# Kernel tuning notes

Measured on AMD Instinct MI355X. Metric: run time of the kernel, lower is better.

Reference implementation:

```python
import jax, jax.numpy as jnp
import numpy as np

T, B, V, NG, H, MLP = 1024, 128, 128, 10, 1024, 128
F = V + NG  # feature_size = alphabet one-hot + genre one-hot


def setup_inputs() -> dict:
    key = jax.random.key(0)
    ks = jax.random.split(key, 14)
    s = 0.02
    inp = {
        "x": jax.random.normal(ks[0], (T, B, F), dtype=jnp.float32),
        # LSTMCell 1: input F -> hidden H (PyTorch layout: W_ih [4H, F], W_hh [4H, H])
        "W_ih1": jax.random.normal(ks[1], (4 * H, F), dtype=jnp.float32) * s,
        "b_ih1": jax.random.normal(ks[2], (4 * H,), dtype=jnp.float32) * s,
        "W_hh1": jax.random.normal(ks[3], (4 * H, H), dtype=jnp.float32) * s,
        "b_hh1": jax.random.normal(ks[4], (4 * H,), dtype=jnp.float32) * s,
        # LSTMCell 2: H -> H
        "W_ih2": jax.random.normal(ks[5], (4 * H, H), dtype=jnp.float32) * s,
        "b_ih2": jax.random.normal(ks[6], (4 * H,), dtype=jnp.float32) * s,
        "W_hh2": jax.random.normal(ks[7], (4 * H, H), dtype=jnp.float32) * s,
        "b_hh2": jax.random.normal(ks[8], (4 * H,), dtype=jnp.float32) * s,
        # MLP head: Linear(H,128) -> SELU -> Linear(128, V). Dropout(0.2) is identity in eval.
        "W1": jax.random.normal(ks[9], (MLP, H), dtype=jnp.float32) * s,
        "b1": jax.random.normal(ks[10], (MLP,), dtype=jnp.float32) * s,
        "W2": jax.random.normal(ks[11], (V, MLP), dtype=jnp.float32) * s,
        "b2": jax.random.normal(ks[12], (V,), dtype=jnp.float32) * s,
        "predict": 0,
    }
    return inp


def _lstm_cell(xt, h, c, W_ih, b_ih, W_hh, b_hh):
    # PyTorch LSTMCell gate order: input, forget, cell(g), output
    gates = xt @ W_ih.T + b_ih + h @ W_hh.T + b_hh  # [B, 4H]
    i, f, g, o = jnp.split(gates, 4, axis=-1)
    i, f, o = jax.nn.sigmoid(i), jax.nn.sigmoid(f), jax.nn.sigmoid(o)
    g = jnp.tanh(g)
    c_new = f * c + i * g
    h_new = o * jnp.tanh(c_new)
    return h_new, c_new


def reference(x, W_ih1, b_ih1, W_hh1, b_hh1, W_ih2, b_ih2, W_hh2, b_hh2,
              W1, b1, W2, b2, predict):
    n = x.shape[1]
    h0 = jnp.zeros((n, H), dtype=jnp.float32)
    init = (h0, h0, h0, h0)  # h_t, c_t, h2_t, c2_t

    def step(carry, xt):
        h, c, h2, c2 = carry
        h, c = _lstm_cell(xt, h, c, W_ih1, b_ih1, W_hh1, b_hh1)
        h2, c2 = _lstm_cell(h, h2, c2, W_ih2, b_ih2, W_hh2, b_hh2)
        out = jax.nn.selu(h2 @ W1.T + b1) @ W2.T + b2  # [B, V]
        return (h, c, h2, c2), out

    _, outputs = jax.lax.scan(step, init, x)  # [T, B, V]
    return outputs
```

## Files before the change

### kernel.cpp

```cpp
#include <hip/hip_runtime.h>
#include <cstdint>
#include <cstddef>

#define TT   1024
#define BB   128
#define FEAT 138
#define FPAD 160
#define HH   1024
#define VV   128
#define MM   128
#define K1   1184
#define K1P  1280
#define K2   2048
#define HCH  1024
#define H1N  131072
#define MIDN 16384
#define PKM1 1032
#define PKM2 136
#define OFF_RED 0
#define OFF_WM  32768
#define OFF_H   65792
#define OFF_M   67840
#define LDSZ    68864

typedef __bf16 bf16x8 __attribute__((ext_vector_type(8)));
typedef float  f32x4  __attribute__((ext_vector_type(4)));
typedef unsigned short u16;

__device__ __forceinline__ u16 f2bf(float f) {
  uint32_t u = __float_as_uint(f);
  u += 0x7fffu + ((u >> 16) & 1u);
  return (u16)(u >> 16);
}
__device__ __forceinline__ float sigm(float x) { return 1.0f / (1.0f + __expf(-x)); }
__device__ __forceinline__ float tanh_(float x) {
  float e = __expf(-2.0f * fabsf(x));
  float t = (1.0f - e) / (1.0f + e);
  return x < 0.0f ? -t : t;
}

__device__ __forceinline__ bf16x8 ldcc8(const u16* p) {
  union { unsigned long long q[2]; bf16x8 v; } u;
  const unsigned long long* p64 = (const unsigned long long*)p;
  u.q[0] = __hip_atomic_load(p64,     __ATOMIC_RELAXED, __HIP_MEMORY_SCOPE_AGENT);
  u.q[1] = __hip_atomic_load(p64 + 1, __ATOMIC_RELAXED, __HIP_MEMORY_SCOPE_AGENT);
  return u.v;
}
__device__ __forceinline__ void stcc16(u16* p, uint4 v) {
  unsigned long long* p64 = (unsigned long long*)p;
  unsigned long long lo = ((unsigned long long)v.y << 32) | v.x;
  unsigned long long hi = ((unsigned long long)v.w << 32) | v.z;
  __hip_atomic_store(p64,     lo, __ATOMIC_RELAXED, __HIP_MEMORY_SCOPE_AGENT);
  __hip_atomic_store(p64 + 1, hi, __ATOMIC_RELAXED, __HIP_MEMORY_SCOPE_AGENT);
}

__global__ void conv_w1i(const float* __restrict__ Wih, const float* __restrict__ Whh,
                         const float* __restrict__ bi, const float* __restrict__ bh,
                         u16* __restrict__ dst, float* __restrict__ bsum) {
  int rp = blockIdx.x;
  int hc = rp >> 2, g = rp & 3;
  int sr = g * HH + hc;
  if (threadIdx.x == 0) bsum[rp] = bi[sr] + bh[sr];
  for (int k = threadIdx.x; k < K1P; k += 256) {
    float v = 0.0f;
    if (k < FPAD)    v = (k < FEAT) ? Wih[(size_t)sr * FEAT + k] : 0.0f;
    else if (k < K1) v = Whh[(size_t)sr * HH + (k - FPAD)];
    dst[(size_t)rp * K1P + k] = f2bf(v);
  }
}
__global__ void conv_w2i(const float* __restrict__ Wih, const float* __restrict__ Whh,
                         const float* __restrict__ bi, const float* __restrict__ bh,
                         u16* __restrict__ dst, float* __restrict__ bsum) {
  int rp = blockIdx.x;
  int hc = rp >> 2, g = rp & 3;
  int sr = g * HH + hc;
  if (threadIdx.x == 0) bsum[rp] = bi[sr] + bh[sr];
  for (int k = threadIdx.x; k < K2; k += 256) {
    float v = (k < HH) ? Wih[(size_t)sr * HH + k] : Whh[(size_t)sr * HH + (k - HH)];
    dst[(size_t)rp * K2 + k] = f2bf(v);
  }
}
__global__ void conv_mlpw(const float* __restrict__ W1, const float* __restrict__ W2,
                          u16* __restrict__ A, u16* __restrict__ Bm) {
  int i = blockIdx.x * 256 + threadIdx.x;
  if (i < MM * HH) A[i] = f2bf(W1[i]);
  else {
    int j = i - MM * HH;
    if (j < VV * MM) Bm[j] = f2bf(W2[j]);
  }
}
__global__ void conv_x(const float* __restrict__ x, u16* __restrict__ Xb) {
  int blk = blockIdx.x;
  int t = blk / 20, c = blk % 20;
  int b = threadIdx.x;
  if (b >= BB) return;
  const float* src = x + ((size_t)t * BB + b) * FEAT;
  u16 v[8];
#pragma unroll
  for (int e = 0; e < 8; ++e) {
    int col = c * 8 + e;
    v[e] = (col < FEAT) ? f2bf(src[col]) : (u16)0;
  }
  *(uint4*)(Xb + (((size_t)t * 20 + c) * BB + b) * 8) = *(uint4*)v;
}
__global__ void zero_ws(uint4* __restrict__ p, int n16) {
  int i = blockIdx.x * 256 + threadIdx.x;
  if (i < n16) p[i] = uint4{0, 0, 0, 0};
}


__device__ __forceinline__ void mac_step(const bf16x8& a0, const bf16x8& a1,
                                         const u16* __restrict__ bptr,
                                         f32x4 (&acc)[2][4]) {
  bf16x8 Bf[4];
#pragma unroll
  for (int n = 0; n < 4; ++n) Bf[n] = *(const bf16x8*)(bptr + n * 128);
#pragma unroll
  for (int n = 0; n < 4; ++n) {
    acc[0][n] = __builtin_amdgcn_mfma_f32_16x16x32_bf16(a0, Bf[n], acc[0][n], 0, 0, 0);
    acc[1][n] = __builtin_amdgcn_mfma_f32_16x16x32_bf16(a1, Bf[n], acc[1][n], 0, 0, 0);
  }
}

__device__ __forceinline__ void ld_tile_cc(const u16* bptr, bf16x8 (&B)[4]) {
#pragma unroll
  for (int n = 0; n < 4; ++n) B[n] = ldcc8(bptr + n * 128);
}
__device__ __forceinline__ void mfma_tile(const bf16x8& a0, const bf16x8& a1,
                                          const bf16x8 (&B)[4], f32x4 (&acc)[2][4]) {
#pragma unroll
  for (int n = 0; n < 4; ++n) {
    acc[0][n] = __builtin_amdgcn_mfma_f32_16x16x32_bf16(a0, B[n], acc[0][n], 0, 0, 0);
    acc[1][n] = __builtin_amdgcn_mfma_f32_16x16x32_bf16(a1, B[n], acc[1][n], 0, 0, 0);
  }
}
template<int NT, int OFS, int NA>
__device__ __forceinline__ void mac_ring_cc(const bf16x8 (&A0)[NA], const bf16x8 (&A1)[NA],
                                            const u16* __restrict__ bp,
                                            f32x4 (&acc)[2][4]) {
  constexpr int D = NT < 4 ? NT : 4;
  bf16x8 Bq[D][4];
#pragma unroll
  for (int s = 0; s < D; ++s) ld_tile_cc(bp + (size_t)s * 4096, Bq[s]);
#pragma unroll
  for (int s = 0; s < NT; ++s) {
    mfma_tile(A0[OFS + s], A1[OFS + s], Bq[s % D], acc);
    if (s + D < NT) ld_tile_cc(bp + (size_t)(s + D) * 4096, Bq[s % D]);
  }
}

__device__ __forceinline__ void red_write(float* __restrict__ rg,
                                          const f32x4 (&acc)[2][4], int lane) {
#pragma unroll
  for (int mt = 0; mt < 2; ++mt)
#pragma unroll
    for (int n = 0; n < 4; ++n)
      *(f32x4*)(rg + (mt * 4 + n) * 256 + lane * 4) = acc[mt][n];
}
__device__ __forceinline__ void red_add(const float* __restrict__ rg,
                                        f32x4 (&acc)[2][4], int lane) {
#pragma unroll
  for (int mt = 0; mt < 2; ++mt)
#pragma unroll
    for (int n = 0; n < 4; ++n)
      acc[mt][n] += *(const f32x4*)(rg + (mt * 4 + n) * 256 + lane * 4);
}

__device__ __forceinline__ void lstm_tail(f32x4 (&acc)[2][4], const f32x4& bsv0,
                                          const f32x4& bsv1, float (&cst)[2][4],
                                          char* smem, int bh, int lane, int q, int l16,
                                          u16* __restrict__ houtChunk) {
  u16* st = (u16*)(smem + OFF_H) + bh * 512;
#pragma unroll
  for (int mt = 0; mt < 2; ++mt) {
    const f32x4 bsv = mt ? bsv1 : bsv0;
#pragma unroll
    for (int n = 0; n < 4; ++n) {
      float iv = sigm(acc[mt][n][0] + bsv[0]);
      float fv = sigm(acc[mt][n][1] + bsv[1]);
      float gv = tanh_(acc[mt][n][2] + bsv[2]);
      float ov = sigm(acc[mt][n][3] + bsv[3]);
      float c = fv * cst[mt][n] + iv * gv;
      cst[mt][n] = c;
      st[(n * 16 + l16) * 8 + mt * 4 + q] = f2bf(ov * tanh_(c));
    }
  }
  uint4 hv4 = *(uint4*)((u16*)(smem + OFF_H) + bh * 512 + lane * 8);
  stcc16(houtChunk + ((size_t)bh * 64 + lane) * 8, hv4);
}

__device__ __forceinline__ void gbar(unsigned* __restrict__ bar, unsigned g) {
  asm volatile("s_waitcnt vmcnt(0)" ::: "memory");
  __syncthreads();
  if (threadIdx.x == 0) {
    unsigned v = __hip_atomic_fetch_add(&bar[(blockIdx.x & 7) * 16], 1u,
                                        __ATOMIC_RELAXED, __HIP_MEMORY_SCOPE_AGENT);
    if (v == 32u * g - 1u) {
      unsigned w = __hip_atomic_fetch_add(&bar[128], 1u,
                                          __ATOMIC_RELAXED, __HIP_MEMORY_SCOPE_AGENT);
      if (w == 8u * g - 1u)
        __hip_atomic_store(&bar[144], g, __ATOMIC_RELAXED, __HIP_MEMORY_SCOPE_AGENT);
    }
    while (__hip_atomic_load(&bar[144], __ATOMIC_RELAXED,
                             __HIP_MEMORY_SCOPE_AGENT) < g)
      __builtin_amdgcn_s_sleep(8);
  }
  __syncthreads();
}

__global__ __launch_bounds__(512, 2) void fused_lstm(
    const u16* __restrict__ W1i, const u16* __restrict__ W2i,
    const u16* __restrict__ W1m, const u16* __restrict__ W2m,
    const u16* __restrict__ Xb, u16* __restrict__ h1b, u16* __restrict__ h2b,
    u16* __restrict__ midb,
    const float* __restrict__ bs1, const float* __restrict__ bs2,
    const float* __restrict__ bm1, const float* __restrict__ bm2,
    float* __restrict__ out, unsigned* __restrict__ bar)
{
  extern __shared__ char smem[];
  const int tid = threadIdx.x, bid = blockIdx.x;
  const int w = tid >> 6, lane = tid & 63, q = lane >> 4, l16 = lane & 15;
  const int kw = w & 3, bh = w >> 2;
  const bool isL1 = bid < 128;
  const int j = isL1 ? bid : bid - 128;
  float* red = (float*)(smem + OFF_RED);
  u16* Wm = (u16*)(smem + OFF_WM);

  float cst[2][4] = {{0, 0, 0, 0}, {0, 0, 0, 0}};
  f32x4 bsv0 = {0, 0, 0, 0}, bsv1 = {0, 0, 0, 0};
  if (kw == 0) {
    const float* bs = isL1 ? bs1 : bs2;
    bsv0 = *(const f32x4*)(bs + (j * 8 + q) * 4);
    bsv1 = *(const f32x4*)(bs + (j * 8 + 4 + q) * 4);
  }

  if (isL1) {
    bf16x8 A1[2][10];
#pragma unroll
    for (int mt = 0; mt < 2; ++mt)
#pragma unroll
      for (int s = 0; s < 10; ++s)
        A1[mt][s] = *(const bf16x8*)(W1i + (size_t)(j * 32 + mt * 16 + l16) * K1P +
                                     (size_t)(kw * 10 + s) * 32 + q * 8);
    if (j < 64) {
      int m0 = (j & 7) * 16;
      for (int i = tid; i < 16 * 128; i += 512) {
        int r = i >> 7, c8 = i & 127;
        *(uint4*)(Wm + r * PKM1 + c8 * 8) =
            *(const uint4*)(W1m + ((size_t)(m0 + r)) * HH + c8 * 8);
      }
    } else {
      int v0 = ((j - 64) & 7) * 16;
      for (int i = tid; i < 16 * 16; i += 512) {
        int r = i >> 4, c8 = i & 15;
        *(uint4*)(Wm + r * PKM2 + c8 * 8) =
            *(const uint4*)(W2m + ((size_t)(v0 + r)) * MM + c8 * 8);
      }
    }
    f32x4 bmv = {0, 0, 0, 0};
    if (w == 3) {
      if (j < 64) bmv = *(const f32x4*)(bm1 + (j & 7) * 16 + q * 4);
      else        bmv = *(const f32x4*)(bm2 + ((j - 64) & 7) * 16 + q * 4);
    }
    __syncthreads();

    for (int p = 0; p < TT + 3; ++p) {
      const bool act = p < TT;
      if (act) {
        const u16* h1p = h1b + (size_t)((p - 1) & 1) * H1N;
        f32x4 acc[2][4];
#pragma unroll
        for (int mt = 0; mt < 2; ++mt)
#pragma unroll
          for (int n = 0; n < 4; ++n) acc[mt][n] = (f32x4){0, 0, 0, 0};
        if (kw == 0) {
          const u16* bx = Xb + (size_t)p * 20480 +
                          ((size_t)q * 128 + bh * 64 + l16) * 8;
#pragma unroll
          for (int s = 0; s < 5; ++s)
            mac_step(A1[0][s], A1[1][s], bx + (size_t)s * 4096, acc);
          const u16* bp = h1p + ((size_t)q * 128 + bh * 64 + l16) * 8;
          mac_ring_cc<5, 5, 10>(A1[0], A1[1], bp, acc);
        } else {
          const u16* bp = h1p + ((size_t)((kw * 10 - 5) * 4 + q) * 128 +
                                 bh * 64 + l16) * 8;
          mac_ring_cc<10, 0, 10>(A1[0], A1[1], bp, acc);
        }
        if (kw >= 2) red_write(red + (bh * 2 + kw - 2) * 2048, acc, lane);
        __syncthreads();
        if (kw < 2)  red_add(red + (bh * 2 + kw) * 2048, acc, lane);
        if (kw == 1) red_write(red + (bh * 2 + 1) * 2048, acc, lane);
        __syncthreads();
        if (kw == 0) {
          red_add(red + (bh * 2 + 1) * 2048, acc, lane);
          lstm_tail(acc, bsv0, bsv1, cst, smem, bh, lane, q, l16,
                    h1b + (size_t)(p & 1) * H1N + (size_t)j * HCH);
        }
      }
      if (w == 3) {
        if (j < 64) {
          if (p >= 2 && p <= TT + 1) {
            int jm = j & 7, jb = j >> 3;
            const u16* bsrc = h2b + (size_t)(p & 1) * H1N + q * HCH +
                              (jb * 16 + l16) * 8;
            const u16* am = Wm + l16 * PKM1 + q * 8;
            f32x4 acc = {0, 0, 0, 0};
            bf16x8 Bq[8];
#pragma unroll
            for (int s = 0; s < 8; ++s) Bq[s] = ldcc8(bsrc + (size_t)s * 4096);
#pragma unroll
            for (int s = 0; s < 32; ++s) {
              bf16x8 af = *(const bf16x8*)(am + s * 32);
              acc = __builtin_amdgcn_mfma_f32_16x16x32_bf16(af, Bq[s % 8], acc, 0, 0, 0);
              if (s + 8 < 32) Bq[s % 8] = ldcc8(bsrc + (size_t)(s + 8) * 4096);
            }
            const float SC = 1.0507009873554804934193349852946f;
            const float AL = 1.6732632423543772848170429916717f;
            u16* st16 = (u16*)(smem + OFF_M);
#pragma unroll
            for (int r = 0; r < 4; ++r) {
              float v = acc[r] + bmv[r];
              v = v > 0.0f ? SC * v : SC * AL * (__expf(v) - 1.0f);
              st16[l16 * 16 + q * 4 + r] = f2bf(v);
            }
            if (lane < 16) {
              uint4 v0 = *(uint4*)(st16 + lane * 16);
              uint4 v1 = *(uint4*)(st16 + lane * 16 + 8);
              u16* mc = midb + (size_t)(p & 1) * MIDN;
              stcc16(mc + (size_t)(2 * jm) * HCH + (jb * 16 + lane) * 8, v0);
              stcc16(mc + (size_t)(2 * jm + 1) * HCH + (jb * 16 + lane) * 8, v1);
            }
          }
        } else if (p >= 3) {
          int jj = j - 64, jv = jj & 7, jb = jj >> 3;
          const u16* bsrc = midb + (size_t)((p - 3) & 1) * MIDN + q * HCH +
                            (jb * 16 + l16) * 8;
          const u16* am = Wm + l16 * PKM2 + q * 8;
          f32x4 acc = {0, 0, 0, 0};
          bf16x8 Bq[4];
#pragma unroll
          for (int s = 0; s < 4; ++s) Bq[s] = ldcc8(bsrc + (size_t)s * 4096);
#pragma unroll
          for (int s = 0; s < 4; ++s) {
            bf16x8 af = *(const bf16x8*)(am + s * 32);
            acc = __builtin_amdgcn_mfma_f32_16x16x32_bf16(af, Bq[s], acc, 0, 0, 0);
          }
          float* stf = (float*)(smem + OFF_M);
#pragma unroll
          for (int r = 0; r < 4; ++r) stf[l16 * 16 + q * 4 + r] = acc[r] + bmv[r];
          if (lane < 16) {
            float* orow = out + ((size_t)(p - 3) * BB + jb * 16 + lane) * VV + jv * 16;
            uint4* s4 = (uint4*)(stf + lane * 16);
            *(uint4*)(orow + 0)  = s4[0];
            *(uint4*)(orow + 4)  = s4[1];
            *(uint4*)(orow + 8)  = s4[2];
            *(uint4*)(orow + 12) = s4[3];
          }
        }
      }
      gbar(bar, (unsigned)p + 1u);
    }
  } else {
    bf16x8 A2[2][16];
#pragma unroll
    for (int mt = 0; mt < 2; ++mt)
#pragma unroll
      for (int s = 0; s < 16; ++s)
        A2[mt][s] = *(const bf16x8*)(W2i + (size_t)(j * 32 + mt * 16 + l16) * K2 +
                                     (size_t)(kw * 16 + s) * 32 + q * 8);

    for (int p = 0; p < TT + 3; ++p) {
      const bool act = (p >= 1 && p <= TT);
      if (act) {
        const int t = p - 1;
        const u16* h1c = h1b + (size_t)(t & 1) * H1N;
        const u16* h2p = h2b + (size_t)((t - 1) & 1) * H1N;
        const u16* src = (kw < 2) ? h1c : h2p;
        const u16* bbase = src + ((size_t)((kw & 1) * 64 + q) * 128 +
                                  bh * 64 + l16) * 8;
        f32x4 acc[2][4];
#pragma unroll
        for (int mt = 0; mt < 2; ++mt)
#pragma unroll
          for (int n = 0; n < 4; ++n) acc[mt][n] = (f32x4){0, 0, 0, 0};
        mac_ring_cc<16, 0, 16>(A2[0], A2[1], bbase, acc);

        if (kw >= 2) red_write(red + (bh * 2 + kw - 2) * 2048, acc, lane);
        __syncthreads();
        if (kw < 2)  red_add(red + (bh * 2 + kw) * 2048, acc, lane);
        if (kw == 1) red_write(red + (bh * 2 + 1) * 2048, acc, lane);
        __syncthreads();
        if (kw == 0) {
          red_add(red + (bh * 2 + 1) * 2048, acc, lane);
          lstm_tail(acc, bsv0, bsv1, cst, smem, bh, lane, q, l16,
                    h2b + (size_t)(t & 1) * H1N + (size_t)j * HCH);
        }
      }
      gbar(bar, (unsigned)p + 1u);
    }
  }
}

extern "C" void kernel_launch(void* const* d_in, const int* in_sizes, int n_in,
                              void* d_out, int out_size, void* d_ws, size_t ws_size,
                              hipStream_t stream)
{
  const float* x    = (const float*)d_in[0];
  const float* Wih1 = (const float*)d_in[1];
  const float* bih1 = (const float*)d_in[2];
  const float* Whh1 = (const float*)d_in[3];
  const float* bhh1 = (const float*)d_in[4];
  const float* Wih2 = (const float*)d_in[5];
  const float* bih2 = (const float*)d_in[6];
  const float* Whh2 = (const float*)d_in[7];
  const float* bhh2 = (const float*)d_in[8];
  const float* W1   = (const float*)d_in[9];
  const float* b1   = (const float*)d_in[10];
  const float* W2   = (const float*)d_in[11];
  const float* b2   = (const float*)d_in[12];
  float* out = (float*)d_out;
  (void)in_sizes; (void)n_in; (void)out_size;

  char* ws = (char*)d_ws;
  size_t off = 0;
  auto alloc = [&](size_t n) { char* p = ws + off; off += (n + 255) & ~(size_t)255; return p; };
  u16* W1i   = (u16*)alloc((size_t)4096 * K1P * 2);
  u16* W2i   = (u16*)alloc((size_t)4096 * K2 * 2);
  u16* W1m   = (u16*)alloc((size_t)MM * HH * 2);
  u16* W2m   = (u16*)alloc((size_t)VV * MM * 2);
  u16* Xb    = (u16*)alloc((size_t)TT * 20 * BB * 8 * 2);
  float* bs1 = (float*)alloc(4096 * 4);
  float* bs2 = (float*)alloc(4096 * 4);
  u16* h1b   = (u16*)alloc(2 * (size_t)H1N * 2 + 32768);
  u16* h2b   = (u16*)alloc(2 * (size_t)H1N * 2);
  u16* midb  = (u16*)alloc(2 * (size_t)MIDN * 2);
  unsigned* bar = (unsigned*)alloc(4096);
  if (ws_size < off) return;

  conv_w1i<<<4096, 256, 0, stream>>>(Wih1, Whh1, bih1, bhh1, W1i, bs1);
  conv_w2i<<<4096, 256, 0, stream>>>(Wih2, Whh2, bih2, bhh2, W2i, bs2);
  conv_mlpw<<<576, 256, 0, stream>>>(W1, W2, W1m, W2m);
  conv_x<<<TT * 20, 128, 0, stream>>>(x, Xb);
  {
    int n16 = (int)((2 * (size_t)H1N * 2 + 32768 + 2 * (size_t)H1N * 2 +
                     2 * (size_t)MIDN * 2 + 4096) / 16);
    zero_ws<<<(n16 + 255) / 256, 256, 0, stream>>>((uint4*)h1b, n16);
  }

  (void)hipFuncSetAttribute((const void*)fused_lstm,
                            hipFuncAttributeMaxDynamicSharedMemorySize, LDSZ);
  void* args[] = { (void*)&W1i, (void*)&W2i, (void*)&W1m, (void*)&W2m,
                   (void*)&Xb, (void*)&h1b, (void*)&h2b, (void*)&midb,
                   (void*)&bs1, (void*)&bs2, (void*)&b1, (void*)&b2,
                   (void*)&out, (void*)&bar };
  hipError_t err = hipLaunchCooperativeKernel((const void*)fused_lstm,
                                              dim3(256), dim3(512), args, LDSZ, stream);
  if (err != hipSuccess) {
    fused_lstm<<<dim3(256), dim3(512), LDSZ, stream>>>(W1i, W2i, W1m, W2m, Xb,
                                                       h1b, h2b, midb, bs1, bs2,
                                                       b1, b2, out, bar);
  }
}
```

Measured before the change: 16.16 ms.

## Move MLP head out of recurrent loop into batched post-kernel and relax loads

When the workspace is large enough, layer-2 hidden states for every timestep are kept in a full history buffer. The MLP head then runs afterwards as a separate batched kernel with one block per timestep, which takes it off the critical path and cuts the recurrent loop from TT+3 to TT+1 barrier phases. The per-step agent-scope atomic loads of shared hidden state become plain vector loads, with an acquire fence added in the grid barrier and a shorter sleep in its spin loop. Layer-1 also trims the tail warp's padded K tiles. The trade-off is a large extra workspace, plus reliance on the fence for cross-block visibility now that the loads are non-atomic.

```diff
diff --git a/kernel.cpp b/kernel.cpp
--- a/kernel.cpp
+++ b/kernel.cpp
@@ -39,13 +39,6 @@
   return x < 0.0f ? -t : t;
 }
 
-__device__ __forceinline__ bf16x8 ldcc8(const u16* p) {
-  union { unsigned long long q[2]; bf16x8 v; } u;
-  const unsigned long long* p64 = (const unsigned long long*)p;
-  u.q[0] = __hip_atomic_load(p64,     __ATOMIC_RELAXED, __HIP_MEMORY_SCOPE_AGENT);
-  u.q[1] = __hip_atomic_load(p64 + 1, __ATOMIC_RELAXED, __HIP_MEMORY_SCOPE_AGENT);
-  return u.v;
-}
 __device__ __forceinline__ void stcc16(u16* p, uint4 v) {
   unsigned long long* p64 = (unsigned long long*)p;
   unsigned long long lo = ((unsigned long long)v.y << 32) | v.x;
@@ -109,44 +102,38 @@
 }
 
 
+__device__ __forceinline__ void mfma_tile(const bf16x8& a0, const bf16x8& a1,
+                                          const bf16x8 (&B)[4], f32x4 (&acc)[2][4]) {
+#pragma unroll
+  for (int n = 0; n < 4; ++n) {
+    acc[0][n] = __builtin_amdgcn_mfma_f32_16x16x32_bf16(a0, B[n], acc[0][n], 0, 0, 0);
+    acc[1][n] = __builtin_amdgcn_mfma_f32_16x16x32_bf16(a1, B[n], acc[1][n], 0, 0, 0);
+  }
+}
+__device__ __forceinline__ void ld_tile(const u16* __restrict__ p, bf16x8 (&B)[4]) {
+#pragma unroll
+  for (int n = 0; n < 4; ++n) B[n] = *(const bf16x8*)(p + n * 128);
+}
+template<int NT, int OFS, int NA>
+__device__ __forceinline__ void mac_ring(const bf16x8 (&A0)[NA], const bf16x8 (&A1)[NA],
+                                         const u16* __restrict__ bp,
+                                         f32x4 (&acc)[2][4]) {
+  constexpr int D = NT < 4 ? NT : 4;
+  bf16x8 Bq[D][4];
+#pragma unroll
+  for (int s = 0; s < D; ++s) ld_tile(bp + (size_t)s * 4096, Bq[s]);
+#pragma unroll
+  for (int s = 0; s < NT; ++s) {
+    mfma_tile(A0[OFS + s], A1[OFS + s], Bq[s % D], acc);
+    if (s + D < NT) ld_tile(bp + (size_t)(s + D) * 4096, Bq[s % D]);
+  }
+}
 __device__ __forceinline__ void mac_step(const bf16x8& a0, const bf16x8& a1,
                                          const u16* __restrict__ bptr,
                                          f32x4 (&acc)[2][4]) {
   bf16x8 Bf[4];
-#pragma unroll
-  for (int n = 0; n < 4; ++n) Bf[n] = *(const bf16x8*)(bptr + n * 128);
-#pragma unroll
-  for (int n = 0; n < 4; ++n) {
-    acc[0][n] = __builtin_amdgcn_mfma_f32_16x16x32_bf16(a0, Bf[n], acc[0][n], 0, 0, 0);
-    acc[1][n] = __builtin_amdgcn_mfma_f32_16x16x32_bf16(a1, Bf[n], acc[1][n], 0, 0, 0);
-  }
-}
-
-__device__ __forceinline__ void ld_tile_cc(const u16* bptr, bf16x8 (&B)[4]) {
-#pragma unroll
-  for (int n = 0; n < 4; ++n) B[n] = ldcc8(bptr + n * 128);
-}
-__device__ __forceinline__ void mfma_tile(const bf16x8& a0, const bf16x8& a1,
-                                          const bf16x8 (&B)[4], f32x4 (&acc)[2][4]) {
-#pragma unroll
-  for (int n = 0; n < 4; ++n) {
-    acc[0][n] = __builtin_amdgcn_mfma_f32_16x16x32_bf16(a0, B[n], acc[0][n], 0, 0, 0);
-    acc[1][n] = __builtin_amdgcn_mfma_f32_16x16x32_bf16(a1, B[n], acc[1][n], 0, 0, 0);
-  }
-}
-template<int NT, int OFS, int NA>
-__device__ __forceinline__ void mac_ring_cc(const bf16x8 (&A0)[NA], const bf16x8 (&A1)[NA],
-                                            const u16* __restrict__ bp,
-                                            f32x4 (&acc)[2][4]) {
-  constexpr int D = NT < 4 ? NT : 4;
-  bf16x8 Bq[D][4];
-#pragma unroll
-  for (int s = 0; s < D; ++s) ld_tile_cc(bp + (size_t)s * 4096, Bq[s]);
-#pragma unroll
-  for (int s = 0; s < NT; ++s) {
-    mfma_tile(A0[OFS + s], A1[OFS + s], Bq[s % D], acc);
-    if (s + D < NT) ld_tile_cc(bp + (size_t)(s + D) * 4096, Bq[s % D]);
-  }
+  ld_tile(bptr, Bf);
+  mfma_tile(a0, a1, Bf, acc);
 }
 
 __device__ __forceinline__ void red_write(float* __restrict__ rg,
@@ -201,18 +188,20 @@
       if (w == 8u * g - 1u)
         __hip_atomic_store(&bar[144], g, __ATOMIC_RELAXED, __HIP_MEMORY_SCOPE_AGENT);
     }
+    __builtin_amdgcn_fence(__ATOMIC_ACQUIRE, "agent");
     while (__hip_atomic_load(&bar[144], __ATOMIC_RELAXED,
                              __HIP_MEMORY_SCOPE_AGENT) < g)
-      __builtin_amdgcn_s_sleep(8);
+      __builtin_amdgcn_s_sleep(1);
   }
   __syncthreads();
 }
 
+template<int MODE>
 __global__ __launch_bounds__(512, 2) void fused_lstm(
     const u16* __restrict__ W1i, const u16* __restrict__ W2i,
     const u16* __restrict__ W1m, const u16* __restrict__ W2m,
     const u16* __restrict__ Xb, u16* __restrict__ h1b, u16* __restrict__ h2b,
-    u16* __restrict__ midb,
+    u16* __restrict__ h2h, u16* __restrict__ midb,
     const float* __restrict__ bs1, const float* __restrict__ bs2,
     const float* __restrict__ bm1, const float* __restrict__ bm2,
     float* __restrict__ out, unsigned* __restrict__ bar)
@@ -225,6 +214,7 @@
   const int j = isL1 ? bid : bid - 128;
   float* red = (float*)(smem + OFF_RED);
   u16* Wm = (u16*)(smem + OFF_WM);
+  const int PEND = MODE ? (TT + 1) : (TT + 3);
 
   float cst[2][4] = {{0, 0, 0, 0}, {0, 0, 0, 0}};
   f32x4 bsv0 = {0, 0, 0, 0}, bsv1 = {0, 0, 0, 0};
@@ -242,29 +232,31 @@
       for (int s = 0; s < 10; ++s)
         A1[mt][s] = *(const bf16x8*)(W1i + (size_t)(j * 32 + mt * 16 + l16) * K1P +
                                      (size_t)(kw * 10 + s) * 32 + q * 8);
-    if (j < 64) {
-      int m0 = (j & 7) * 16;
-      for (int i = tid; i < 16 * 128; i += 512) {
-        int r = i >> 7, c8 = i & 127;
-        *(uint4*)(Wm + r * PKM1 + c8 * 8) =
-            *(const uint4*)(W1m + ((size_t)(m0 + r)) * HH + c8 * 8);
+    f32x4 bmv = {0, 0, 0, 0};
+    if constexpr (MODE == 0) {
+      if (j < 64) {
+        int m0 = (j & 7) * 16;
+        for (int i = tid; i < 16 * 128; i += 512) {
+          int r = i >> 7, c8 = i & 127;
+          *(uint4*)(Wm + r * PKM1 + c8 * 8) =
+              *(const uint4*)(W1m + ((size_t)(m0 + r)) * HH + c8 * 8);
+        }
+      } else {
+        int v0 = ((j - 64) & 7) * 16;
+        for (int i = tid; i < 16 * 16; i += 512) {
+          int r = i >> 4, c8 = i & 15;
+          *(uint4*)(Wm + r * PKM2 + c8 * 8) =
+              *(const uint4*)(W2m + ((size_t)(v0 + r)) * MM + c8 * 8);
+        }
       }
-    } else {
-      int v0 = ((j - 64) & 7) * 16;
-      for (int i = tid; i < 16 * 16; i += 512) {
-        int r = i >> 4, c8 = i & 15;
-        *(uint4*)(Wm + r * PKM2 + c8 * 8) =
-            *(const uint4*)(W2m + ((size_t)(v0 + r)) * MM + c8 * 8);
+      if (w == 3) {
+        if (j < 64) bmv = *(const f32x4*)(bm1 + (j & 7) * 16 + q * 4);
+        else        bmv = *(const f32x4*)(bm2 + ((j - 64) & 7) * 16 + q * 4);
       }
-    }
-    f32x4 bmv = {0, 0, 0, 0};
-    if (w == 3) {
-      if (j < 64) bmv = *(const f32x4*)(bm1 + (j & 7) * 16 + q * 4);
-      else        bmv = *(const f32x4*)(bm2 + ((j - 64) & 7) * 16 + q * 4);
-    }
-    __syncthreads();
-
-    for (int p = 0; p < TT + 3; ++p) {
+      __syncthreads();
+    }
+
+    for (int p = 0; p < PEND; ++p) {
       const bool act = p < TT;
       if (act) {
         const u16* h1p = h1b + (size_t)((p - 1) & 1) * H1N;
@@ -276,15 +268,14 @@
         if (kw == 0) {
           const u16* bx = Xb + (size_t)p * 20480 +
                           ((size_t)q * 128 + bh * 64 + l16) * 8;
-#pragma unroll
-          for (int s = 0; s < 5; ++s)
-            mac_step(A1[0][s], A1[1][s], bx + (size_t)s * 4096, acc);
+          mac_ring<5, 0, 10>(A1[0], A1[1], bx, acc);
           const u16* bp = h1p + ((size_t)q * 128 + bh * 64 + l16) * 8;
-          mac_ring_cc<5, 5, 10>(A1[0], A1[1], bp, acc);
+          mac_ring<5, 5, 10>(A1[0], A1[1], bp, acc);
         } else {
           const u16* bp = h1p + ((size_t)((kw * 10 - 5) * 4 + q) * 128 +
                                  bh * 64 + l16) * 8;
-          mac_ring_cc<10, 0, 10>(A1[0], A1[1], bp, acc);
+          if (kw == 3) mac_ring<7, 0, 10>(A1[0], A1[1], bp, acc);
+          else         mac_ring<10, 0, 10>(A1[0], A1[1], bp, acc);
         }
         if (kw >= 2) red_write(red + (bh * 2 + kw - 2) * 2048, acc, lane);
         __syncthreads();
@@ -297,64 +288,61 @@
                     h1b + (size_t)(p & 1) * H1N + (size_t)j * HCH);
         }
       }
-      if (w == 3) {
-        if (j < 64) {
-          if (p >= 2 && p <= TT + 1) {
-            int jm = j & 7, jb = j >> 3;
-            const u16* bsrc = h2b + (size_t)(p & 1) * H1N + q * HCH +
+      if constexpr (MODE == 0) {
+        if (w == 3) {
+          if (j < 64) {
+            if (p >= 2 && p <= TT + 1) {
+              int jm = j & 7, jb = j >> 3;
+              const u16* bsrc = h2b + (size_t)(p & 1) * H1N + q * HCH +
+                                (jb * 16 + l16) * 8;
+              const u16* am = Wm + l16 * PKM1 + q * 8;
+              f32x4 acc = {0, 0, 0, 0};
+#pragma unroll 4
+              for (int s = 0; s < 32; ++s) {
+                bf16x8 bf = *(const bf16x8*)(bsrc + (size_t)s * 4096);
+                bf16x8 af = *(const bf16x8*)(am + s * 32);
+                acc = __builtin_amdgcn_mfma_f32_16x16x32_bf16(af, bf, acc, 0, 0, 0);
+              }
+              const float SC = 1.0507009873554804934193349852946f;
+              const float AL = 1.6732632423543772848170429916717f;
+              u16* st16 = (u16*)(smem + OFF_M);
+#pragma unroll
+              for (int r = 0; r < 4; ++r) {
+                float v = acc[r] + bmv[r];
+                v = v > 0.0f ? SC * v : SC * AL * (__expf(v) - 1.0f);
+                st16[l16 * 16 + q * 4 + r] = f2bf(v);
+              }
+              if (lane < 16) {
+                uint4 v0 = *(uint4*)(st16 + lane * 16);
+                uint4 v1 = *(uint4*)(st16 + lane * 16 + 8);
+                u16* mc = midb + (size_t)(p & 1) * MIDN;
+                stcc16(mc + (size_t)(2 * jm) * HCH + (jb * 16 + lane) * 8, v0);
+                stcc16(mc + (size_t)(2 * jm + 1) * HCH + (jb * 16 + lane) * 8, v1);
+              }
+            }
+          } else if (p >= 3) {
+            int jj = j - 64, jv = jj & 7, jb = jj >> 3;
+            const u16* bsrc = midb + (size_t)((p - 3) & 1) * MIDN + q * HCH +
                               (jb * 16 + l16) * 8;
-            const u16* am = Wm + l16 * PKM1 + q * 8;
+            const u16* am = Wm + l16 * PKM2 + q * 8;
             f32x4 acc = {0, 0, 0, 0};
-            bf16x8 Bq[8];
-#pragma unroll
-            for (int s = 0; s < 8; ++s) Bq[s] = ldcc8(bsrc + (size_t)s * 4096);
-#pragma unroll
-            for (int s = 0; s < 32; ++s) {
+#pragma unroll
+            for (int s = 0; s < 4; ++s) {
+              bf16x8 bf = *(const bf16x8*)(bsrc + (size_t)s * 4096);
               bf16x8 af = *(const bf16x8*)(am + s * 32);
-              acc = __builtin_amdgcn_mfma_f32_16x16x32_bf16(af, Bq[s % 8], acc, 0, 0, 0);
-              if (s + 8 < 32) Bq[s % 8] = ldcc8(bsrc + (size_t)(s + 8) * 4096);
+              acc = __builtin_amdgcn_mfma_f32_16x16x32_bf16(af, bf, acc, 0, 0, 0);
             }
-            const float SC = 1.0507009873554804934193349852946f;
-            const float AL = 1.6732632423543772848170429916717f;
-            u16* st16 = (u16*)(smem + OFF_M);
-#pragma unroll
-            for (int r = 0; r < 4; ++r) {
-              float v = acc[r] + bmv[r];
-              v = v > 0.0f ? SC * v : SC * AL * (__expf(v) - 1.0f);
-              st16[l16 * 16 + q * 4 + r] = f2bf(v);
+            float* stf = (float*)(smem + OFF_M);
+#pragma unroll
+            for (int r = 0; r < 4; ++r) stf[l16 * 16 + q * 4 + r] = acc[r] + bmv[r];
+            if (lane < 16) {
+              float* orow = out + ((size_t)(p - 3) * BB + jb * 16 + lane) * VV + jv * 16;
+              uint4* s4 = (uint4*)(stf + lane * 16);
+              *(uint4*)(orow + 0)  = s4[0];
+              *(uint4*)(orow + 4)  = s4[1];
+              *(uint4*)(orow + 8)  = s4[2];
+              *(uint4*)(orow + 12) = s4[3];
             }
-            if (lane < 16) {
-              uint4 v0 = *(uint4*)(st16 + lane * 16);
-              uint4 v1 = *(uint4*)(st16 + lane * 16 + 8);
-              u16* mc = midb + (size_t)(p & 1) * MIDN;
-              stcc16(mc + (size_t)(2 * jm) * HCH + (jb * 16 + lane) * 8, v0);
-              stcc16(mc + (size_t)(2 * jm + 1) * HCH + (jb * 16 + lane) * 8, v1);
-            }
-          }
-        } else if (p >= 3) {
-          int jj = j - 64, jv = jj & 7, jb = jj >> 3;
-          const u16* bsrc = midb + (size_t)((p - 3) & 1) * MIDN + q * HCH +
-                            (jb * 16 + l16) * 8;
-          const u16* am = Wm + l16 * PKM2 + q * 8;
-          f32x4 acc = {0, 0, 0, 0};
-          bf16x8 Bq[4];
-#pragma unroll
-          for (int s = 0; s < 4; ++s) Bq[s] = ldcc8(bsrc + (size_t)s * 4096);
-#pragma unroll
-          for (int s = 0; s < 4; ++s) {
-            bf16x8 af = *(const bf16x8*)(am + s * 32);
-            acc = __builtin_amdgcn_mfma_f32_16x16x32_bf16(af, Bq[s], acc, 0, 0, 0);
-          }
-          float* stf = (float*)(smem + OFF_M);
-#pragma unroll
-          for (int r = 0; r < 4; ++r) stf[l16 * 16 + q * 4 + r] = acc[r] + bmv[r];
-          if (lane < 16) {
-            float* orow = out + ((size_t)(p - 3) * BB + jb * 16 + lane) * VV + jv * 16;
-            uint4* s4 = (uint4*)(stf + lane * 16);
-            *(uint4*)(orow + 0)  = s4[0];
-            *(uint4*)(orow + 4)  = s4[1];
-            *(uint4*)(orow + 8)  = s4[2];
-            *(uint4*)(orow + 12) = s4[3];
           }
         }
       }
@@ -369,12 +357,13 @@
         A2[mt][s] = *(const bf16x8*)(W2i + (size_t)(j * 32 + mt * 16 + l16) * K2 +
                                      (size_t)(kw * 16 + s) * 32 + q * 8);
 
-    for (int p = 0; p < TT + 3; ++p) {
+    for (int p = 0; p < PEND; ++p) {
       const bool act = (p >= 1 && p <= TT);
       if (act) {
         const int t = p - 1;
         const u16* h1c = h1b + (size_t)(t & 1) * H1N;
-        const u16* h2p = h2b + (size_t)((t - 1) & 1) * H1N;
+        const u16* h2p = MODE ? (h2h + (size_t)t * H1N)
+                              : (h2b + (size_t)((t - 1) & 1) * H1N);
         const u16* src = (kw < 2) ? h1c : h2p;
         const u16* bbase = src + ((size_t)((kw & 1) * 64 + q) * 128 +
                                   bh * 64 + l16) * 8;
@@ -383,7 +372,7 @@
         for (int mt = 0; mt < 2; ++mt)
 #pragma unroll
           for (int n = 0; n < 4; ++n) acc[mt][n] = (f32x4){0, 0, 0, 0};
-        mac_ring_cc<16, 0, 16>(A2[0], A2[1], bbase, acc);
+        mac_ring<16, 0, 16>(A2[0], A2[1], bbase, acc);
 
         if (kw >= 2) red_write(red + (bh * 2 + kw - 2) * 2048, acc, lane);
         __syncthreads();
@@ -392,13 +381,92 @@
         __syncthreads();
         if (kw == 0) {
           red_add(red + (bh * 2 + 1) * 2048, acc, lane);
-          lstm_tail(acc, bsv0, bsv1, cst, smem, bh, lane, q, l16,
-                    h2b + (size_t)(t & 1) * H1N + (size_t)j * HCH);
+          u16* dst = MODE ? (h2h + (size_t)(t + 1) * H1N + (size_t)j * HCH)
+                          : (h2b + (size_t)(t & 1) * H1N + (size_t)j * HCH);
+          lstm_tail(acc, bsv0, bsv1, cst, smem, bh, lane, q, l16, dst);
         }
       }
       gbar(bar, (unsigned)p + 1u);
     }
   }
+}
+
+__global__ __launch_bounds__(256) void mlp_head(
+    const u16* __restrict__ W1m, const u16* __restrict__ W2m,
+    const u16* __restrict__ h2h, const float* __restrict__ b1,
+    const float* __restrict__ b2, float* __restrict__ out)
+{
+  __shared__ u16 midl[16 * 128 * 8];
+  const int tid = threadIdx.x, t = blockIdx.x;
+  const int wid = tid >> 6, lane = tid & 63, q = lane >> 4, l16 = lane & 15;
+  const u16* h2t = h2h + (size_t)(t + 1) * H1N;
+  const int mbase = wid * 32;
+
+  f32x4 acc[2][8];
+#pragma unroll
+  for (int a = 0; a < 2; ++a)
+#pragma unroll
+    for (int n = 0; n < 8; ++n) acc[a][n] = (f32x4){0, 0, 0, 0};
+#pragma unroll 2
+  for (int kc = 0; kc < 32; ++kc) {
+    bf16x8 a0 = *(const bf16x8*)(W1m + (size_t)(mbase + l16) * HH + kc * 32 + q * 8);
+    bf16x8 a1 = *(const bf16x8*)(W1m + (size_t)(mbase + 16 + l16) * HH + kc * 32 + q * 8);
+    const u16* bp = h2t + (size_t)(kc * 4 + q) * 1024 + l16 * 8;
+#pragma unroll
+    for (int n = 0; n < 8; ++n) {
+      bf16x8 bf = *(const bf16x8*)(bp + n * 128);
+      acc[0][n] = __builtin_amdgcn_mfma_f32_16x16x32_bf16(a0, bf, acc[0][n], 0, 0, 0);
+      acc[1][n] = __builtin_amdgcn_mfma_f32_16x16x32_bf16(a1, bf, acc[1][n], 0, 0, 0);
+    }
+  }
+  const float SC = 1.0507009873554804934193349852946f;
+  const float AL = 1.6732632423543772848170429916717f;
+  f32x4 bm0 = *(const f32x4*)(b1 + mbase + q * 4);
+  f32x4 bm1v = *(const f32x4*)(b1 + mbase + 16 + q * 4);
+#pragma unroll
+  for (int mt = 0; mt < 2; ++mt) {
+    const f32x4 bm = mt ? bm1v : bm0;
+    const int m0 = mbase + mt * 16 + q * 4;
+#pragma unroll
+    for (int n = 0; n < 8; ++n) {
+      const int b = n * 16 + l16;
+#pragma unroll
+      for (int r = 0; r < 4; ++r) {
+        float v = acc[mt][n][r] + bm[r];
+        v = v > 0.0f ? SC * v : SC * AL * (__expf(v) - 1.0f);
+        int mm = m0 + r;
+        midl[(mm >> 3) * 1024 + b * 8 + (mm & 7)] = f2bf(v);
+      }
+    }
+  }
+  __syncthreads();
+  f32x4 acc2[2][8];
+#pragma unroll
+  for (int a = 0; a < 2; ++a)
+#pragma unroll
+    for (int n = 0; n < 8; ++n) acc2[a][n] = (f32x4){0, 0, 0, 0};
+#pragma unroll
+  for (int kc = 0; kc < 4; ++kc) {
+    bf16x8 a0 = *(const bf16x8*)(W2m + (size_t)(mbase + l16) * MM + kc * 32 + q * 8);
+    bf16x8 a1 = *(const bf16x8*)(W2m + (size_t)(mbase + 16 + l16) * MM + kc * 32 + q * 8);
+    const u16* bp = midl + (kc * 4 + q) * 1024 + l16 * 8;
+#pragma unroll
+    for (int n = 0; n < 8; ++n) {
+      bf16x8 bf = *(const bf16x8*)(bp + n * 128);
+      acc2[0][n] = __builtin_amdgcn_mfma_f32_16x16x32_bf16(a0, bf, acc2[0][n], 0, 0, 0);
+      acc2[1][n] = __builtin_amdgcn_mfma_f32_16x16x32_bf16(a1, bf, acc2[1][n], 0, 0, 0);
+    }
+  }
+  f32x4 c0 = *(const f32x4*)(b2 + mbase + q * 4);
+  f32x4 c1 = *(const f32x4*)(b2 + mbase + 16 + q * 4);
+  float* ot = out + (size_t)t * BB * VV;
+#pragma unroll
+  for (int mt = 0; mt < 2; ++mt)
+#pragma unroll
+    for (int n = 0; n < 8; ++n) {
+      f32x4 v = acc2[mt][n] + (mt ? c1 : c0);
+      *(f32x4*)(ot + (size_t)(n * 16 + l16) * VV + mbase + mt * 16 + q * 4) = v;
+    }
 }
 
 extern "C" void kernel_launch(void* const* d_in, const int* in_sizes, int n_in,
@@ -435,7 +503,10 @@
   u16* h2b   = (u16*)alloc(2 * (size_t)H1N * 2);
   u16* midb  = (u16*)alloc(2 * (size_t)MIDN * 2);
   unsigned* bar = (unsigned*)alloc(4096);
-  if (ws_size < off) return;
+  size_t off_base = off;
+  u16* h2h   = (u16*)alloc((size_t)(TT + 1) * H1N * 2);
+  const bool postMLP = ws_size >= off;
+  if (ws_size < off_base) return;
 
   conv_w1i<<<4096, 256, 0, stream>>>(Wih1, Whh1, bih1, bhh1, W1i, bs1);
   conv_w2i<<<4096, 256, 0, stream>>>(Wih2, Whh2, bih2, bhh2, W2i, bs2);
@@ -446,18 +517,31 @@
                      2 * (size_t)MIDN * 2 + 4096) / 16);
     zero_ws<<<(n16 + 255) / 256, 256, 0, stream>>>((uint4*)h1b, n16);
   }
-
-  (void)hipFuncSetAttribute((const void*)fused_lstm,
+  if (postMLP) {
+    zero_ws<<<(H1N * 2 / 16 + 255) / 256, 256, 0, stream>>>((uint4*)h2h, H1N * 2 / 16);
+  }
+
+  using KFn = void (*)(const u16*, const u16*, const u16*, const u16*, const u16*,
+                       u16*, u16*, u16*, u16*, const float*, const float*,
+                       const float*, const float*, float*, unsigned*);
+  KFn fp = postMLP ? (KFn)fused_lstm<1> : (KFn)fused_lstm<0>;
+  (void)hipFuncSetAttribute((const void*)fp,
                             hipFuncAttributeMaxDynamicSharedMemorySize, LDSZ);
   void* args[] = { (void*)&W1i, (void*)&W2i, (void*)&W1m, (void*)&W2m,
-                   (void*)&Xb, (void*)&h1b, (void*)&h2b, (void*)&midb,
+                   (void*)&Xb, (void*)&h1b, (void*)&h2b, (void*)&h2h, (void*)&midb,
                    (void*)&bs1, (void*)&bs2, (void*)&b1, (void*)&b2,
                    (void*)&out, (void*)&bar };
-  hipError_t err = hipLaunchCooperativeKernel((const void*)fused_lstm,
+  hipError_t err = hipLaunchCooperativeKernel((const void*)fp,
                                               dim3(256), dim3(512), args, LDSZ, stream);
   if (err != hipSuccess) {
-    fused_lstm<<<dim3(256), dim3(512), LDSZ, stream>>>(W1i, W2i, W1m, W2m, Xb,
-                                                       h1b, h2b, midb, bs1, bs2,
-                                                       b1, b2, out, bar);
-  }
-}
+    if (postMLP)
+      fused_lstm<1><<<dim3(256), dim3(512), LDSZ, stream>>>(
+          W1i, W2i, W1m, W2m, Xb, h1b, h2b, h2h, midb, bs1, bs2, b1, b2, out, bar);
+    else
+      fused_lstm<0><<<dim3(256), dim3(512), LDSZ, stream>>>(
+          W1i, W2i, W1m, W2m, Xb, h1b, h2b, h2h, midb, bs1, bs2, b1, b2, out, bar);
+  }
+  if (postMLP) {
+    mlp_head<<<dim3(TT), dim3(256), 0, stream>>>(W1m, W2m, h2h, b1, b2, out);
+  }
+}
```

After: 14.72 ms. 8.9% less time.
